# Optimization experiments

Hardware: AMD Instinct MI355X
Metric: run time of the kernel (lower is better)

## Reference

```python
import jax, jax.numpy as jnp
import numpy as np

B = 524288   # number of samples scored at inference
K = 8        # GMM mixture components
D = 16       # latent feature dim (AE code + reconstruction-error features)


def setup_inputs() -> dict:
    key = jax.random.key(0)
    k1, k2, k3, k4 = jax.random.split(key, 4)
    z = jax.random.normal(k1, (B, D), dtype=jnp.float32)
    mu = jax.random.normal(k2, (K, D), dtype=jnp.float32)
    # sigma must be SPD (it is an estimated covariance + 0.001*I in the original);
    # build it as A A^T / D + 0.1*I so cholesky succeeds and densities are sane.
    A = jax.random.normal(k3, (K, D, D), dtype=jnp.float32) / np.sqrt(D)
    sigma = jnp.einsum('kij,klj->kil', A, A) + 0.1 * jnp.eye(D, dtype=jnp.float32)
    logits = jax.random.normal(k4, (K,), dtype=jnp.float32)
    mixture_probabilities = jax.nn.softmax(logits)
    return {"mu": mu, "sigma": sigma, "z": z,
            "mixture_probabilities": mixture_probabilities}


def reference(mu, sigma, z, mixture_probabilities):
    # Faithful to compute_sample_energy: per-sample MVN density for each of K
    # components via Cholesky, weighted by mixture probs, summed, -log.
    # Vectorized: one batched triangular solve instead of tf.map_fn per sample.
    d = z.shape[-1]
    L = jnp.linalg.cholesky(sigma)                      # [K,D,D]
    diff = z[:, None, :] - mu[None, :, :]               # [B,K,D]
    diff_t = jnp.transpose(diff, (1, 2, 0))             # [K,D,B]
    y = jax.scipy.linalg.solve_triangular(L, diff_t, lower=True)  # [K,D,B]
    maha = jnp.sum(y * y, axis=1)                       # [K,B] Mahalanobis dist
    log_det = jnp.sum(jnp.log(jnp.diagonal(L, axis1=-2, axis2=-1)), axis=-1)  # [K]
    log_norm = -0.5 * d * jnp.log(jnp.asarray(2.0 * np.pi, dtype=z.dtype))
    log_prob = log_norm - log_det[:, None] - 0.5 * maha  # [K,B]
    densities = jnp.exp(log_prob).T                      # [B,K] == map_fn(prob)
    energy = -jnp.log(jnp.sum(densities * mixture_probabilities, axis=1))  # [B]
    return energy
```

## Files before the change

### kernel.cpp

```cpp
#include <hip/hip_runtime.h>
#include <math.h>

#define KCOMP 8
#define DDIM  16

typedef __attribute__((ext_vector_type(8))) short bf16x8;
typedef __attribute__((ext_vector_type(4))) float f32x4;

static __device__ __forceinline__ short f2bf(float f) {
    unsigned u = __float_as_uint(f);
    unsigned r = (u + 0x7FFFu + ((u >> 16) & 1u)) >> 16;
    return (short)r;
}


__global__ __launch_bounds__(128) void prep_kernel(
    const float* __restrict__ mu, const float* __restrict__ sigma,
    const float* __restrict__ pi, float* __restrict__ ws)
{
    __shared__ float sLinv[KCOMP * DDIM * DDIM];
    const int tid = threadIdx.x;
    const int g = tid >> 4;
    const int r = tid & 15;

    float a[DDIM];
    const float4* srow = (const float4*)(sigma + g * DDIM * DDIM + r * DDIM);
    float4 v0 = srow[0], v1 = srow[1], v2 = srow[2], v3 = srow[3];
    a[0]=v0.x;  a[1]=v0.y;  a[2]=v0.z;  a[3]=v0.w;
    a[4]=v1.x;  a[5]=v1.y;  a[6]=v1.z;  a[7]=v1.w;
    a[8]=v2.x;  a[9]=v2.y;  a[10]=v2.z; a[11]=v2.w;
    a[12]=v3.x; a[13]=v3.y; a[14]=v3.z; a[15]=v3.w;

    float l[DDIM];
    #pragma unroll
    for (int j = 0; j < DDIM; ++j) {
        float s = a[j];
        #pragma unroll
        for (int m = 0; m < j; ++m)
            s -= l[m] * __shfl(l[m], j, DDIM);
        float dj = sqrtf(__shfl(s, j, DDIM));
        float val;
        if (r == j)      val = dj;
        else if (r > j)  val = s / dj;
        else             val = 0.0f;
        l[j] = val;
    }

    float x[DDIM];
    #pragma unroll
    for (int i = 0; i < DDIM; ++i) {
        float t = (r == i) ? 1.0f : 0.0f;
        #pragma unroll
        for (int m = 0; m < i; ++m)
            t -= __shfl(l[m], i, DDIM) * x[m];
        x[i] = t / __shfl(l[i], i, DDIM);
    }

    #pragma unroll
    for (int i = 0; i < DDIM; ++i) {
        sLinv[g * 256 + i * DDIM + r] = x[i];
        ws[g * 256 + i * DDIM + r]    = x[i];
    }
    __syncthreads();

    float b = 0.0f;
    #pragma unroll
    for (int c = 0; c < DDIM; ++c)
        b += sLinv[g * 256 + r * DDIM + c] * mu[g * DDIM + c];
    ws[KCOMP * 256 + g * DDIM + r] = b;

    float ld = logf(l[r]);
    #pragma unroll
    for (int off = 8; off >= 1; off >>= 1)
        ld += __shfl_xor(ld, off, DDIM);
    if (r == 0) {
        const float LOG2PI = 1.8378770664093454f;
        float ck = logf(pi[g]) - ld - 0.5f * DDIM * LOG2PI;
        ws[KCOMP * 256 + KCOMP * DDIM + g] = ck;
    }
}

__global__ __launch_bounds__(256) void energy_kernel(
    const float* __restrict__ z, const float* __restrict__ ws,
    float* __restrict__ out, int n)
{
    const int lane = threadIdx.x & 63;
    const int m    = lane & 15;
    const int quad = lane >> 4;
    const int wave = (blockIdx.x * blockDim.x + threadIdx.x) >> 6;

    bf16x8 afrag[KCOMP];
    #pragma unroll
    for (int k = 0; k < KCOMP; ++k) {
        bf16x8 a = {0,0,0,0,0,0,0,0};
        if (quad < 2) {
            const float* Lrow = ws + k * 256 + m * DDIM + quad * 8;
            #pragma unroll
            for (int j = 0; j < 8; ++j) a[j] = f2bf(Lrow[j]);
        } else if (quad == 2) {
            a[0] = f2bf(-ws[KCOMP * 256 + k * DDIM + m]);
        }
        afrag[k] = a;
    }
    float ck[KCOMP];
    #pragma unroll
    for (int k = 0; k < KCOMP; ++k)
        ck[k] = ws[KCOMP * 256 + KCOMP * DDIM + k];

    const f32x4 zero4 = {0.f, 0.f, 0.f, 0.f};
    const int SPW = 256;
    const int base = wave * SPW;

    #pragma unroll 1
    for (int it = 0; it < SPW / 64; ++it) {
        const int tb = base + it * 64;
        float en[4];
        #pragma unroll
        for (int t = 0; t < 4; ++t) {
            bf16x8 bfrag = {0,0,0,0,0,0,0,0};
            const int s = tb + t * 16 + m;
            if (quad < 2) {
                if (s < n) {
                    const float* zp = z + (size_t)s * DDIM + quad * 8;
                    #pragma unroll
                    for (int j = 0; j < 8; ++j) bfrag[j] = f2bf(zp[j]);
                }
            } else if (quad == 2) {
                bfrag[0] = (short)0x3F80;
            }

            f32x4 dres[KCOMP];
            #pragma unroll
            for (int k = 0; k < KCOMP; ++k)
                dres[k] = __builtin_amdgcn_mfma_f32_16x16x32_bf16(
                              afrag[k], bfrag, zero4, 0, 0, 0);

            float mx = -1e30f, dens = 0.0f;
            #pragma unroll
            for (int k = 0; k < KCOMP; ++k) {
                f32x4 d4 = dres[k];
                float p = d4[0]*d4[0] + d4[1]*d4[1] + d4[2]*d4[2] + d4[3]*d4[3];
                p += __shfl_xor(p, 16, 64);
                p += __shfl_xor(p, 32, 64);
                float lp = fmaf(-0.5f, p, ck[k]);
                float nm = fmaxf(mx, lp);
                dens = dens * __expf(mx - nm) + __expf(lp - nm);
                mx = nm;
            }
            en[t] = -(mx + __logf(dens));
        }
        float e = en[0];
        e = (quad == 1) ? en[1] : e;
        e = (quad == 2) ? en[2] : e;
        e = (quad == 3) ? en[3] : e;
        const int so = tb + quad * 16 + m;
        if (so < n) out[so] = e;
    }
}

extern "C" void kernel_launch(void* const* d_in, const int* in_sizes, int n_in,
                              void* d_out, int out_size, void* d_ws, size_t ws_size,
                              hipStream_t stream) {
    const float* mu    = (const float*)d_in[0];
    const float* sigma = (const float*)d_in[1];
    const float* z     = (const float*)d_in[2];
    const float* pi    = (const float*)d_in[3];
    float* ws  = (float*)d_ws;
    float* out = (float*)d_out;

    const int n = in_sizes[2] / DDIM;

    prep_kernel<<<1, 128, 0, stream>>>(mu, sigma, pi, ws);

    const int blocks = (n + 1023) / 1024;
    energy_kernel<<<blocks, 256, 0, stream>>>(z, ws, out, n);
}
```

Before: 106.4 us.

## Fuse Cholesky prep into energy kernel and compute logsumexp once per sample

Every block now redoes the Cholesky factorization and triangular inverse of the 8 covariances in shared memory, so the separate prep launch and its global workspace round-trip go away. The per-sample log-sum-exp is also restructured: the Mahalanobis sums for all four 16-sample tiles are gathered first, each lane selects its own sample, and the exp/log is evaluated once per sample instead of being replicated across all 64 lanes for every tile. The cost is redundant prep work (serial shuffle chains, sqrt and divides) in each of the 512 blocks before any sample work starts, plus a larger register array.

Measured after the change: 113.4 us. +6.5%, slower.

```diff
diff --git a/kernel.cpp b/kernel.cpp
--- a/kernel.cpp
+++ b/kernel.cpp
@@ -13,108 +13,105 @@
     return (short)r;
 }
 
-
-__global__ __launch_bounds__(128) void prep_kernel(
+__global__ __launch_bounds__(256) void dagmm_kernel(
     const float* __restrict__ mu, const float* __restrict__ sigma,
-    const float* __restrict__ pi, float* __restrict__ ws)
+    const float* __restrict__ pi, const float* __restrict__ z,
+    float* __restrict__ out, int n)
 {
     __shared__ float sLinv[KCOMP * DDIM * DDIM];
+    __shared__ float sB[KCOMP * DDIM];
+    __shared__ float sC[KCOMP];
+
     const int tid = threadIdx.x;
-    const int g = tid >> 4;
-    const int r = tid & 15;
 
-    float a[DDIM];
-    const float4* srow = (const float4*)(sigma + g * DDIM * DDIM + r * DDIM);
-    float4 v0 = srow[0], v1 = srow[1], v2 = srow[2], v3 = srow[3];
-    a[0]=v0.x;  a[1]=v0.y;  a[2]=v0.z;  a[3]=v0.w;
-    a[4]=v1.x;  a[5]=v1.y;  a[6]=v1.z;  a[7]=v1.w;
-    a[8]=v2.x;  a[9]=v2.y;  a[10]=v2.z; a[11]=v2.w;
-    a[12]=v3.x; a[13]=v3.y; a[14]=v3.z; a[15]=v3.w;
+    if (tid < 128) {
+        const int g = tid >> 4;
+        const int r = tid & 15;
 
-    float l[DDIM];
-    #pragma unroll
-    for (int j = 0; j < DDIM; ++j) {
-        float s = a[j];
+        float a[DDIM];
+        const float4* srow = (const float4*)(sigma + g * DDIM * DDIM + r * DDIM);
+        float4 v0 = srow[0], v1 = srow[1], v2 = srow[2], v3 = srow[3];
+        a[0]=v0.x;  a[1]=v0.y;  a[2]=v0.z;  a[3]=v0.w;
+        a[4]=v1.x;  a[5]=v1.y;  a[6]=v1.z;  a[7]=v1.w;
+        a[8]=v2.x;  a[9]=v2.y;  a[10]=v2.z; a[11]=v2.w;
+        a[12]=v3.x; a[13]=v3.y; a[14]=v3.z; a[15]=v3.w;
+
+        float l[DDIM];
         #pragma unroll
-        for (int m = 0; m < j; ++m)
-            s -= l[m] * __shfl(l[m], j, DDIM);
-        float dj = sqrtf(__shfl(s, j, DDIM));
-        float val;
-        if (r == j)      val = dj;
-        else if (r > j)  val = s / dj;
-        else             val = 0.0f;
-        l[j] = val;
-    }
+        for (int j = 0; j < DDIM; ++j) {
+            float s = a[j];
+            #pragma unroll
+            for (int m2 = 0; m2 < j; ++m2)
+                s -= l[m2] * __shfl(l[m2], j, DDIM);
+            float dj = sqrtf(__shfl(s, j, DDIM));
+            float val;
+            if (r == j)      val = dj;
+            else if (r > j)  val = s / dj;
+            else             val = 0.0f;
+            l[j] = val;
+        }
 
-    float x[DDIM];
-    #pragma unroll
-    for (int i = 0; i < DDIM; ++i) {
-        float t = (r == i) ? 1.0f : 0.0f;
+        float x[DDIM];
         #pragma unroll
-        for (int m = 0; m < i; ++m)
-            t -= __shfl(l[m], i, DDIM) * x[m];
-        x[i] = t / __shfl(l[i], i, DDIM);
-    }
+        for (int i = 0; i < DDIM; ++i) {
+            float t = (r == i) ? 1.0f : 0.0f;
+            #pragma unroll
+            for (int m2 = 0; m2 < i; ++m2)
+                t -= __shfl(l[m2], i, DDIM) * x[m2];
+            x[i] = t / __shfl(l[i], i, DDIM);
+        }
 
-    #pragma unroll
-    for (int i = 0; i < DDIM; ++i) {
-        sLinv[g * 256 + i * DDIM + r] = x[i];
-        ws[g * 256 + i * DDIM + r]    = x[i];
+        #pragma unroll
+        for (int i = 0; i < DDIM; ++i)
+            sLinv[g * 256 + i * DDIM + r] = x[i];
+
+        float b = 0.0f;
+        #pragma unroll
+        for (int c = 0; c < DDIM; ++c)
+            b += sLinv[g * 256 + r * DDIM + c] * mu[g * DDIM + c];
+        sB[g * DDIM + r] = b;
+
+        float ld = logf(l[r]);
+        #pragma unroll
+        for (int off = 8; off >= 1; off >>= 1)
+            ld += __shfl_xor(ld, off, DDIM);
+        if (r == 0) {
+            const float LOG2PI = 1.8378770664093454f;
+            sC[g] = logf(pi[g]) - ld - 0.5f * DDIM * LOG2PI;
+        }
     }
     __syncthreads();
 
-    float b = 0.0f;
-    #pragma unroll
-    for (int c = 0; c < DDIM; ++c)
-        b += sLinv[g * 256 + r * DDIM + c] * mu[g * DDIM + c];
-    ws[KCOMP * 256 + g * DDIM + r] = b;
-
-    float ld = logf(l[r]);
-    #pragma unroll
-    for (int off = 8; off >= 1; off >>= 1)
-        ld += __shfl_xor(ld, off, DDIM);
-    if (r == 0) {
-        const float LOG2PI = 1.8378770664093454f;
-        float ck = logf(pi[g]) - ld - 0.5f * DDIM * LOG2PI;
-        ws[KCOMP * 256 + KCOMP * DDIM + g] = ck;
-    }
-}
-
-__global__ __launch_bounds__(256) void energy_kernel(
-    const float* __restrict__ z, const float* __restrict__ ws,
-    float* __restrict__ out, int n)
-{
-    const int lane = threadIdx.x & 63;
+    const int lane = tid & 63;
     const int m    = lane & 15;
     const int quad = lane >> 4;
-    const int wave = (blockIdx.x * blockDim.x + threadIdx.x) >> 6;
+    const int wave = (blockIdx.x * 256 + tid) >> 6;
 
     bf16x8 afrag[KCOMP];
     #pragma unroll
     for (int k = 0; k < KCOMP; ++k) {
         bf16x8 a = {0,0,0,0,0,0,0,0};
         if (quad < 2) {
-            const float* Lrow = ws + k * 256 + m * DDIM + quad * 8;
+            const float* Lrow = &sLinv[k * 256 + m * DDIM + quad * 8];
             #pragma unroll
             for (int j = 0; j < 8; ++j) a[j] = f2bf(Lrow[j]);
         } else if (quad == 2) {
-            a[0] = f2bf(-ws[KCOMP * 256 + k * DDIM + m]);
+            a[0] = f2bf(-sB[k * DDIM + m]);
         }
         afrag[k] = a;
     }
     float ck[KCOMP];
     #pragma unroll
-    for (int k = 0; k < KCOMP; ++k)
-        ck[k] = ws[KCOMP * 256 + KCOMP * DDIM + k];
+    for (int k = 0; k < KCOMP; ++k) ck[k] = sC[k];
 
     const f32x4 zero4 = {0.f, 0.f, 0.f, 0.f};
-    const int SPW = 256;
-    const int base = wave * SPW;
+    const int base = wave * 256;
 
     #pragma unroll 1
-    for (int it = 0; it < SPW / 64; ++it) {
+    for (int it = 0; it < 4; ++it) {
         const int tb = base + it * 64;
-        float en[4];
+        float pk[4][KCOMP];
+
         #pragma unroll
         for (int t = 0; t < 4; ++t) {
             bf16x8 bfrag = {0,0,0,0,0,0,0,0};
@@ -129,32 +126,35 @@
                 bfrag[0] = (short)0x3F80;
             }
 
-            f32x4 dres[KCOMP];
-            #pragma unroll
-            for (int k = 0; k < KCOMP; ++k)
-                dres[k] = __builtin_amdgcn_mfma_f32_16x16x32_bf16(
-                              afrag[k], bfrag, zero4, 0, 0, 0);
-
-            float mx = -1e30f, dens = 0.0f;
             #pragma unroll
             for (int k = 0; k < KCOMP; ++k) {
-                f32x4 d4 = dres[k];
+                f32x4 d4 = __builtin_amdgcn_mfma_f32_16x16x32_bf16(
+                               afrag[k], bfrag, zero4, 0, 0, 0);
                 float p = d4[0]*d4[0] + d4[1]*d4[1] + d4[2]*d4[2] + d4[3]*d4[3];
                 p += __shfl_xor(p, 16, 64);
                 p += __shfl_xor(p, 32, 64);
-                float lp = fmaf(-0.5f, p, ck[k]);
-                float nm = fmaxf(mx, lp);
-                dens = dens * __expf(mx - nm) + __expf(lp - nm);
-                mx = nm;
+                pk[t][k] = p;
             }
-            en[t] = -(mx + __logf(dens));
         }
-        float e = en[0];
-        e = (quad == 1) ? en[1] : e;
-        e = (quad == 2) ? en[2] : e;
-        e = (quad == 3) ? en[3] : e;
+
+        float lp[KCOMP];
+        #pragma unroll
+        for (int k = 0; k < KCOMP; ++k) {
+            float p = pk[0][k];
+            p = (quad == 1) ? pk[1][k] : p;
+            p = (quad == 2) ? pk[2][k] : p;
+            p = (quad == 3) ? pk[3][k] : p;
+            lp[k] = fmaf(-0.5f, p, ck[k]);
+        }
+        float mx = lp[0];
+        #pragma unroll
+        for (int k = 1; k < KCOMP; ++k) mx = fmaxf(mx, lp[k]);
+        float dens = 0.0f;
+        #pragma unroll
+        for (int k = 0; k < KCOMP; ++k) dens += __expf(lp[k] - mx);
+
         const int so = tb + quad * 16 + m;
-        if (so < n) out[so] = e;
+        if (so < n) out[so] = -(mx + __logf(dens));
     }
 }
 
@@ -165,13 +165,11 @@
     const float* sigma = (const float*)d_in[1];
     const float* z     = (const float*)d_in[2];
     const float* pi    = (const float*)d_in[3];
-    float* ws  = (float*)d_ws;
     float* out = (float*)d_out;
+    (void)d_ws; (void)ws_size;
 
     const int n = in_sizes[2] / DDIM;
 
-    prep_kernel<<<1, 128, 0, stream>>>(mu, sigma, pi, ws);
-
     const int blocks = (n + 1023) / 1024;
-    energy_kernel<<<blocks, 256, 0, stream>>>(z, ws, out, n);
+    dagmm_kernel<<<blocks, 256, 0, stream>>>(mu, sigma, pi, z, out, n);
 }
```
